# Performance work log

Hardware: AMD Instinct MI355X
Metric: run time of the kernel (lower is better)

## Reference

```python
import jax, jax.numpy as jnp
import numpy as np

B, C, N, K = 2, 64, 65536, 16
OUT = 64


def setup_inputs() -> dict:
    key = jax.random.key(0)
    k1, k2, k3, k4 = jax.random.split(key, 4)
    x = jax.random.normal(k1, (B, C, N, 1), dtype=jnp.float32)
    edge_index = jax.random.randint(k2, (2, B, N, K), 0, N, dtype=jnp.int64)
    # 1x1 conv weight of MLP2dLayer([2*C, OUT]) and its bias
    W = jax.random.normal(k3, (OUT, 2 * C), dtype=jnp.float32) * (1.0 / np.sqrt(2 * C))
    b = jax.random.normal(k4, (OUT,), dtype=jnp.float32) * 0.01
    return {"x": x, "edge_index": edge_index, "W": W, "b": b}


def reference(x, edge_index, W, b):
    # x: [B, C, N, 1], edge_index: [2, B, N, K]
    Bs, Cs, Ns, _ = x.shape
    Ks = edge_index.shape[-1]
    feat = x[..., 0]                                   # [B, C, N]
    idx = edge_index[0].reshape(Bs, 1, Ns * Ks)        # [B, 1, N*K]
    idx = jnp.broadcast_to(idx, (Bs, Cs, Ns * Ks))
    x_j = jnp.take_along_axis(feat, idx, axis=2).reshape(Bs, Cs, Ns, Ks)  # gather neighbors
    x_i = jnp.broadcast_to(x[..., :1], (Bs, Cs, Ns, Ks))                  # repeated center feature
    msg = jnp.concatenate([x_i, x_j - x_i], axis=1)    # [B, 2C, N, K]
    h = jnp.einsum("oi,bink->bonk", W, msg) + b[None, :, None, None]
    h = jax.nn.relu(h)                                 # MLP2dLayer: 1x1 conv + relu (norm=None)
    out = jnp.max(h, axis=-1, keepdims=True)           # max aggregation over neighbors
    return out
```

## Files before the change

kernel.cpp:

```cpp
#include <hip/hip_runtime.h>


using u32 = unsigned int;
using u16 = unsigned short;
typedef short short8 __attribute__((ext_vector_type(8)));
typedef float f32x4 __attribute__((ext_vector_type(4)));
typedef int i32x4 __attribute__((ext_vector_type(4)));

#define NN 65536

static __device__ __forceinline__ u16 bf16r(float a) {
  u32 u = __builtin_bit_cast(u32, a);
  return (u16)((u + 0x7fffu + ((u >> 16) & 1u)) >> 16);
}
static __device__ __forceinline__ u32 pack_bf16(float a, float b) {
  return (u32)bf16r(a) | ((u32)bf16r(b) << 16);
}
static __device__ __forceinline__ float bf16f(u16 v) {
  u32 u = ((u32)v) << 16;
  return __builtin_bit_cast(float, u);
}

__global__ __launch_bounds__(256) void prep_w(const float* __restrict__ W,
                                              u32* __restrict__ Wcat) {
  int id = blockIdx.x * 256 + threadIdx.x;
  int o = id >> 5, c2 = id & 31;
  float f0, f1;
  if (o < 64) {
    f0 = W[o * 128 + 2 * c2]     - W[o * 128 + 64 + 2 * c2];
    f1 = W[o * 128 + 2 * c2 + 1] - W[o * 128 + 64 + 2 * c2 + 1];
  } else {
    int om = o - 64;
    f0 = W[om * 128 + 64 + 2 * c2];
    f1 = W[om * 128 + 64 + 2 * c2 + 1];
  }
  Wcat[id] = pack_bf16(f0, f1);
}

__global__ __launch_bounds__(256, 4) void k1(const float* __restrict__ x,
                                             const float* __restrict__ bias,
                                             const u32* __restrict__ Wcat,
                                             u16* __restrict__ Ubf,
                                             u16* __restrict__ Vbf) {
  __shared__ __align__(16) char smem[26880];
  u32* Wb = (u32*)smem;
  u32* Xa = (u32*)(smem + 18432);

  int t = threadIdx.x;
  int l = t & 63;
  int w = t >> 6;
  int b = blockIdx.x >> 10;
  int n0 = (blockIdx.x & 1023) << 6;

#pragma unroll
  for (int i = 0; i < 16; ++i) {
    int id = i * 256 + t;
    Wb[(id >> 5) * 36 + (id & 31)] = Wcat[id];
  }
#pragma unroll
  for (int r = 0; r < 8; ++r) {
    int c2 = r * 4 + w;
    size_t base = ((size_t)(b * 64 + 2 * c2)) * NN + n0 + l;
    Xa[l * 33 + c2] = pack_bf16(x[base], x[base + NN]);
  }
  __syncthreads();

  f32x4 acc[8];
#pragma unroll
  for (int f = 0; f < 8; ++f) acc[f] = {0.f, 0.f, 0.f, 0.f};

#pragma unroll
  for (int kb = 0; kb < 2; ++kb) {
    int ar = (16 * w + (l & 15)) * 33 + kb * 16 + 4 * (l >> 4);
    i32x4 av = {(int)Xa[ar], (int)Xa[ar + 1], (int)Xa[ar + 2], (int)Xa[ar + 3]};
    short8 a = __builtin_bit_cast(short8, av);
#pragma unroll
    for (int f = 0; f < 8; ++f) {
      i32x4 bv = *(const i32x4*)(Wb + (16 * f + (l & 15)) * 36 + kb * 16 + 4 * (l >> 4));
      short8 bb = __builtin_bit_cast(short8, bv);
      acc[f] = __builtin_amdgcn_mfma_f32_16x16x32_bf16(a, bb, acc[f], 0, 0, 0);
    }
  }

  float bs[4];
#pragma unroll
  for (int f = 0; f < 4; ++f) bs[f] = bias[16 * f + (l & 15)];

  __syncthreads();
  u16* TR16 = (u16*)smem;
#pragma unroll
  for (int f = 0; f < 4; ++f) {
#pragma unroll
    for (int r = 0; r < 4; ++r) {
      int node = 16 * w + 4 * (l >> 4) + r;
      int o = 16 * f + (l & 15);
      float uval = acc[f][r] + bs[f];
      float vval = acc[f + 4][r];
      TR16[node * 136 + o] = bf16r(uval);
      TR16[node * 136 + 64 + o] = bf16r(vval);
    }
  }
  __syncthreads();

  u32* TR32 = (u32*)smem;
  u32* Up = (u32*)Ubf;
  u32* Vp = (u32*)Vbf;
  int o2 = t & 63;
#pragma unroll
  for (int i = 0; i < 16; ++i) {
    int n = i * 4 + w;
    u32 v = TR32[n * 68 + o2];
    size_t nb = (size_t)(b * NN + n0 + n);
    if (o2 < 32) Up[nb * 32 + o2] = v;
    else         Vp[nb * 32 + (o2 - 32)] = v;
  }
}

__global__ __launch_bounds__(256, 4) void k2(const int* __restrict__ eidx,
                                             const u16* __restrict__ Ubf,
                                             const u16* __restrict__ Vbf,
                                             float* __restrict__ out) {
  __shared__ float tile[64][65];

  int t = threadIdx.x;
  int l = t & 63;
  int w = t >> 6;
  int b = blockIdx.x >> 10;
  int n0 = (blockIdx.x & 1023) << 6;

  const int4* e4 = (const int4*)(eidx + ((size_t)(b * NN) + n0 + w * 16) * 16);
  int4 mi = e4[l];

  const u16* Vb = Vbf + ((size_t)b) * NN * 64 + l;
  const u16* Ub = Ubf + ((size_t)(b * NN) + n0 + w * 16) * 64 + l;

#pragma unroll
  for (int s = 0; s < 16; ++s) {
    int lb = 4 * s;
    int e0 = __builtin_amdgcn_readlane(mi.x, lb);
    int e1 = __builtin_amdgcn_readlane(mi.y, lb);
    int e2 = __builtin_amdgcn_readlane(mi.z, lb);
    int e3 = __builtin_amdgcn_readlane(mi.w, lb);
    int e4_ = __builtin_amdgcn_readlane(mi.x, lb + 1);
    int e5 = __builtin_amdgcn_readlane(mi.y, lb + 1);
    int e6 = __builtin_amdgcn_readlane(mi.z, lb + 1);
    int e7 = __builtin_amdgcn_readlane(mi.w, lb + 1);
    int e8 = __builtin_amdgcn_readlane(mi.x, lb + 2);
    int e9 = __builtin_amdgcn_readlane(mi.y, lb + 2);
    int ea = __builtin_amdgcn_readlane(mi.z, lb + 2);
    int eb = __builtin_amdgcn_readlane(mi.w, lb + 2);
    int ec = __builtin_amdgcn_readlane(mi.x, lb + 3);
    int ed = __builtin_amdgcn_readlane(mi.y, lb + 3);
    int ee = __builtin_amdgcn_readlane(mi.z, lb + 3);
    int ef = __builtin_amdgcn_readlane(mi.w, lb + 3);

    float g0 = bf16f(Vb[(size_t)e0 * 64]);
    float g1 = bf16f(Vb[(size_t)e1 * 64]);
    float g2 = bf16f(Vb[(size_t)e2 * 64]);
    float g3 = bf16f(Vb[(size_t)e3 * 64]);
    float g4 = bf16f(Vb[(size_t)e4_ * 64]);
    float g5 = bf16f(Vb[(size_t)e5 * 64]);
    float g6 = bf16f(Vb[(size_t)e6 * 64]);
    float g7 = bf16f(Vb[(size_t)e7 * 64]);
    float g8 = bf16f(Vb[(size_t)e8 * 64]);
    float g9 = bf16f(Vb[(size_t)e9 * 64]);
    float ga = bf16f(Vb[(size_t)ea * 64]);
    float gb = bf16f(Vb[(size_t)eb * 64]);
    float gc = bf16f(Vb[(size_t)ec * 64]);
    float gd = bf16f(Vb[(size_t)ed * 64]);
    float ge = bf16f(Vb[(size_t)ee * 64]);
    float gf = bf16f(Vb[(size_t)ef * 64]);

    float u = bf16f(Ub[(size_t)s * 64]);

    float m = fmaxf(fmaxf(fmaxf(fmaxf(g0, g1), fmaxf(g2, g3)),
                          fmaxf(fmaxf(g4, g5), fmaxf(g6, g7))),
                    fmaxf(fmaxf(fmaxf(g8, g9), fmaxf(ga, gb)),
                          fmaxf(fmaxf(gc, gd), fmaxf(ge, gf))));

    tile[l][w * 16 + s] = fmaxf(u + m, 0.0f);
  }
  __syncthreads();

#pragma unroll
  for (int r = 0; r < 16; ++r) {
    int o = (r << 2) + (t >> 6);
    int jj = t & 63;
    out[((size_t)(b * 64 + o)) * NN + n0 + jj] = tile[o][jj];
  }
}

extern "C" void kernel_launch(void* const* d_in, const int* in_sizes, int n_in,
                              void* d_out, int out_size, void* d_ws, size_t ws_size,
                              hipStream_t stream) {
  const float* x = (const float*)d_in[0];
  const int* eidx = (const int*)d_in[1];
  const float* W = (const float*)d_in[2];
  const float* bias = (const float*)d_in[3];

  u16* Ubf = (u16*)d_ws;
  u16* Vbf = Ubf + (size_t)2 * NN * 64;
  u32* Wcat = (u32*)((char*)d_ws + (size_t)2 * 2 * NN * 64 * sizeof(u16));

  prep_w<<<16, 256, 0, stream>>>(W, Wcat);
  k1<<<2 * 1024, 256, 0, stream>>>(x, bias, Wcat, Ubf, Vbf);
  k2<<<2 * 1024, 256, 0, stream>>>(eidx, Ubf, Vbf, (float*)d_out);
}
```

Before: 59.97 us.

## Vectorize neighbor gathers in k2 with 16-byte loads and LDS-staged indices

The gather kernel now stages each block's edge indices in shared memory. Instead of each lane loading one bf16 channel per neighbor, groups of 8 lanes each fetch a 16-byte chunk (8 channels) of a neighbor's row, so one wave handles 8 nodes at once. This replaces many 2-byte scattered loads and readlane-driven scalar indexing with fewer, wider memory transactions. It also raises the launch-bounds occupancy hint to 6 blocks, at the cost of more register pressure from the 8 running maxima and some LDS bank traffic on the transposed tile writes.

```diff
diff --git a/kernel.cpp b/kernel.cpp
--- a/kernel.cpp
+++ b/kernel.cpp
@@ -16,9 +16,11 @@
 static __device__ __forceinline__ u32 pack_bf16(float a, float b) {
   return (u32)bf16r(a) | ((u32)bf16r(b) << 16);
 }
-static __device__ __forceinline__ float bf16f(u16 v) {
-  u32 u = ((u32)v) << 16;
-  return __builtin_bit_cast(float, u);
+static __device__ __forceinline__ float bflo(u32 x) {
+  return __builtin_bit_cast(float, x << 16);
+}
+static __device__ __forceinline__ float bfhi(u32 x) {
+  return __builtin_bit_cast(float, x & 0xffff0000u);
 }
 
 __global__ __launch_bounds__(256) void prep_w(const float* __restrict__ W,
@@ -116,10 +118,11 @@
   }
 }
 
-__global__ __launch_bounds__(256, 4) void k2(const int* __restrict__ eidx,
+__global__ __launch_bounds__(256, 6) void k2(const int* __restrict__ eidx,
                                              const u16* __restrict__ Ubf,
                                              const u16* __restrict__ Vbf,
                                              float* __restrict__ out) {
+  __shared__ int eix[1024];
   __shared__ float tile[64][65];
 
   int t = threadIdx.x;
@@ -128,65 +131,51 @@
   int b = blockIdx.x >> 10;
   int n0 = (blockIdx.x & 1023) << 6;
 
-  const int4* e4 = (const int4*)(eidx + ((size_t)(b * NN) + n0 + w * 16) * 16);
-  int4 mi = e4[l];
+  ((int4*)eix)[t] = ((const int4*)(eidx + ((size_t)(b * NN) + n0) * 16))[t];
+  __syncthreads();
 
-  const u16* Vb = Vbf + ((size_t)b) * NN * 64 + l;
-  const u16* Ub = Ubf + ((size_t)(b * NN) + n0 + w * 16) * 64 + l;
+  const int nj = l >> 3;
+  const int c = l & 7;
+  const u16* Vb = Vbf + ((size_t)b) * NN * 64 + c * 8;
 
 #pragma unroll
-  for (int s = 0; s < 16; ++s) {
-    int lb = 4 * s;
-    int e0 = __builtin_amdgcn_readlane(mi.x, lb);
-    int e1 = __builtin_amdgcn_readlane(mi.y, lb);
-    int e2 = __builtin_amdgcn_readlane(mi.z, lb);
-    int e3 = __builtin_amdgcn_readlane(mi.w, lb);
-    int e4_ = __builtin_amdgcn_readlane(mi.x, lb + 1);
-    int e5 = __builtin_amdgcn_readlane(mi.y, lb + 1);
-    int e6 = __builtin_amdgcn_readlane(mi.z, lb + 1);
-    int e7 = __builtin_amdgcn_readlane(mi.w, lb + 1);
-    int e8 = __builtin_amdgcn_readlane(mi.x, lb + 2);
-    int e9 = __builtin_amdgcn_readlane(mi.y, lb + 2);
-    int ea = __builtin_amdgcn_readlane(mi.z, lb + 2);
-    int eb = __builtin_amdgcn_readlane(mi.w, lb + 2);
-    int ec = __builtin_amdgcn_readlane(mi.x, lb + 3);
-    int ed = __builtin_amdgcn_readlane(mi.y, lb + 3);
-    int ee = __builtin_amdgcn_readlane(mi.z, lb + 3);
-    int ef = __builtin_amdgcn_readlane(mi.w, lb + 3);
+  for (int g = 0; g < 2; ++g) {
+    int node = w * 16 + g * 8 + nj;
+    const int4* ep = (const int4*)(eix + node * 16);
+    int4 ea = ep[0], eb = ep[1], ec = ep[2], ed = ep[3];
 
-    float g0 = bf16f(Vb[(size_t)e0 * 64]);
-    float g1 = bf16f(Vb[(size_t)e1 * 64]);
-    float g2 = bf16f(Vb[(size_t)e2 * 64]);
-    float g3 = bf16f(Vb[(size_t)e3 * 64]);
-    float g4 = bf16f(Vb[(size_t)e4_ * 64]);
-    float g5 = bf16f(Vb[(size_t)e5 * 64]);
-    float g6 = bf16f(Vb[(size_t)e6 * 64]);
-    float g7 = bf16f(Vb[(size_t)e7 * 64]);
-    float g8 = bf16f(Vb[(size_t)e8 * 64]);
-    float g9 = bf16f(Vb[(size_t)e9 * 64]);
-    float ga = bf16f(Vb[(size_t)ea * 64]);
-    float gb = bf16f(Vb[(size_t)eb * 64]);
-    float gc = bf16f(Vb[(size_t)ec * 64]);
-    float gd = bf16f(Vb[(size_t)ed * 64]);
-    float ge = bf16f(Vb[(size_t)ee * 64]);
-    float gf = bf16f(Vb[(size_t)ef * 64]);
+    float mx[8];
+#pragma unroll
+    for (int i = 0; i < 8; ++i) mx[i] = -3.0e38f;
 
-    float u = bf16f(Ub[(size_t)s * 64]);
+    auto G = [&](int e) {
+      const uint4 v = *(const uint4*)(Vb + (size_t)e * 64);
+      mx[0] = fmaxf(mx[0], bflo(v.x)); mx[1] = fmaxf(mx[1], bfhi(v.x));
+      mx[2] = fmaxf(mx[2], bflo(v.y)); mx[3] = fmaxf(mx[3], bfhi(v.y));
+      mx[4] = fmaxf(mx[4], bflo(v.z)); mx[5] = fmaxf(mx[5], bfhi(v.z));
+      mx[6] = fmaxf(mx[6], bflo(v.w)); mx[7] = fmaxf(mx[7], bfhi(v.w));
+    };
+    G(ea.x); G(ea.y); G(ea.z); G(ea.w);
+    G(eb.x); G(eb.y); G(eb.z); G(eb.w);
+    G(ec.x); G(ec.y); G(ec.z); G(ec.w);
+    G(ed.x); G(ed.y); G(ed.z); G(ed.w);
 
-    float m = fmaxf(fmaxf(fmaxf(fmaxf(g0, g1), fmaxf(g2, g3)),
-                          fmaxf(fmaxf(g4, g5), fmaxf(g6, g7))),
-                    fmaxf(fmaxf(fmaxf(g8, g9), fmaxf(ga, gb)),
-                          fmaxf(fmaxf(gc, gd), fmaxf(ge, gf))));
-
-    tile[l][w * 16 + s] = fmaxf(u + m, 0.0f);
+    const uint4 uv = *(const uint4*)(Ubf + (((size_t)(b * NN) + n0 + node) << 6) + c * 8);
+    tile[8 * c + 0][node] = fmaxf(bflo(uv.x) + mx[0], 0.f);
+    tile[8 * c + 1][node] = fmaxf(bfhi(uv.x) + mx[1], 0.f);
+    tile[8 * c + 2][node] = fmaxf(bflo(uv.y) + mx[2], 0.f);
+    tile[8 * c + 3][node] = fmaxf(bfhi(uv.y) + mx[3], 0.f);
+    tile[8 * c + 4][node] = fmaxf(bflo(uv.z) + mx[4], 0.f);
+    tile[8 * c + 5][node] = fmaxf(bfhi(uv.z) + mx[5], 0.f);
+    tile[8 * c + 6][node] = fmaxf(bflo(uv.w) + mx[6], 0.f);
+    tile[8 * c + 7][node] = fmaxf(bfhi(uv.w) + mx[7], 0.f);
   }
   __syncthreads();
 
 #pragma unroll
   for (int r = 0; r < 16; ++r) {
-    int o = (r << 2) + (t >> 6);
-    int jj = t & 63;
-    out[((size_t)(b * 64 + o)) * NN + n0 + jj] = tile[o][jj];
+    int o = (r << 2) + w;
+    out[((size_t)(b * 64 + o)) * NN + n0 + l] = tile[o][l];
   }
 }
 
```

After: 65.89 us. 1.1x slower.
